# Performance work log

Measured on AMD Instinct MI355X. Metric: run time of the kernel, lower is better.

## Reference

```python
import jax, jax.numpy as jnp
import numpy as np

B = 32768
N_KPS = 14
DIM = N_KPS * 3   # 42
H1 = 1024
N_DOF = 7

# Fixed kinematic-chain constants (stand-in for the robot's link geometry,
# Franka-like link lengths; constants on device in the original).
LINK_LEN = jnp.array([0.333, 0.316, 0.384, 0.088, 0.107, 0.103, 0.100], dtype=jnp.float32)
OFF = jnp.array([0.05, 0.0, 0.0], dtype=jnp.float32)  # per-link auxiliary keypoint offset


def _rot_z(t):
    c, s = jnp.cos(t), jnp.sin(t)
    z, o = jnp.zeros_like(t), jnp.ones_like(t)
    return jnp.stack([jnp.stack([c, -s, z], -1),
                      jnp.stack([s, c, z], -1),
                      jnp.stack([z, z, o], -1)], -2)


def _rot_y(t):
    c, s = jnp.cos(t), jnp.sin(t)
    z, o = jnp.zeros_like(t), jnp.ones_like(t)
    return jnp.stack([jnp.stack([c, z, s], -1),
                      jnp.stack([z, o, z], -1),
                      jnp.stack([-s, z, c], -1)], -2)


def compute_3n_loss_42_rob(angles):
    """Forward kinematics: angles [B,7] -> keypoints [B,14,3].
    Alternating z/y revolute joints; 2 keypoints per link (origin + offset)."""
    Bn = angles.shape[0]
    R = jnp.broadcast_to(jnp.eye(3, dtype=angles.dtype), (Bn, 3, 3))
    p = jnp.zeros((Bn, 3), dtype=angles.dtype)
    pts = []
    for j in range(N_DOF):
        Rj = _rot_z(angles[:, j]) if j % 2 == 0 else _rot_y(angles[:, j])
        R = jnp.einsum('bij,bjk->bik', R, Rj)
        p = p + R @ jnp.array([0.0, 0.0, 1.0], dtype=angles.dtype) * LINK_LEN[j]
        pts.append(p)
        pts.append(p + R @ OFF)
    return jnp.stack(pts, axis=1)  # [B, 14, 3]


def compute_rede_rt(P, Q):
    """Batched Kabsch: rigid (R, t) minimizing ||R P + t - Q||. P,Q: [B,N,3]."""
    cp = P.mean(axis=1, keepdims=True)
    cq = Q.mean(axis=1, keepdims=True)
    H = jnp.einsum('bni,bnj->bij', P - cp, Q - cq)  # [B,3,3]
    U, S, Vt = jnp.linalg.svd(H)
    V = jnp.swapaxes(Vt, -1, -2)
    d = jnp.sign(jnp.linalg.det(jnp.einsum('bij,bkj->bik', V, U)))
    D = jnp.concatenate([jnp.ones((P.shape[0], 2), P.dtype), d[:, None]], axis=1)
    R = jnp.einsum('bij,bj,bkj->bik', V, D, U)  # V diag(1,1,d) U^T
    t = cq[:, 0] - jnp.einsum('bij,bj->bi', R, cp[:, 0])
    return R, t


def setup_inputs() -> dict:
    key = jax.random.key(0)
    k1, k2, k3, k4, k5 = jax.random.split(key, 5)
    return {
        'joints_3d_pred': jax.random.normal(k1, (B, N_KPS, 3), dtype=jnp.float32),
        'W1': jax.random.normal(k2, (DIM, H1), dtype=jnp.float32) * 0.05,
        'b1': jax.random.normal(k3, (H1,), dtype=jnp.float32) * 0.01,
        'W2': jax.random.normal(k4, (H1, N_DOF), dtype=jnp.float32) * 0.05,
        'b2': jax.random.normal(k5, (N_DOF,), dtype=jnp.float32) * 0.01,
    }


def reference(joints_3d_pred, W1, b1, W2, b2):
    # normalize to root keypoint
    norm = joints_3d_pred - joints_3d_pred[:, :1, :]          # [B,14,3]
    x = norm.reshape(norm.shape[0], -1)                        # [B,42]
    h = jax.nn.relu(x @ W1 + b1)                               # [B,1024]
    angles = h @ W2 + b2                                       # [B,7]
    all_dof_pred = angles[:, :, None]                          # [B,7,1]
    rob = compute_3n_loss_42_rob(angles)                       # [B,14,3]
    R, t = compute_rede_rt(rob, norm)
    t = t + joints_3d_pred[:, 0]                               # un-normalize translation
    top = jnp.concatenate([R, t[:, :, None]], axis=2)          # [B,3,4]
    bottom = jnp.broadcast_to(jnp.array([0.0, 0.0, 0.0, 1.0], dtype=R.dtype), (R.shape[0], 1, 4))
    pose = jnp.concatenate([top, bottom], axis=1)              # [B,4,4]
    return all_dof_pred, pose
```

## Files before the change

### kernel.cpp

```cpp
#include <hip/hip_runtime.h>
#include <math.h>

typedef __attribute__((ext_vector_type(8))) _Float16 half8;
typedef __attribute__((ext_vector_type(4))) _Float16 half4;
typedef __attribute__((ext_vector_type(2))) __fp16   fp16x2;
typedef __attribute__((ext_vector_type(4))) float f32x4;

constexpr int B_   = 32768;
constexpr int NKPS = 14;
constexpr int DIM  = 42;
constexpr int H1_  = 1024;
constexpr int NDOF = 7;

__device__ __forceinline__ void gload_lds16(const _Float16* g, _Float16* l) {
    __builtin_amdgcn_global_load_lds(
        (const __attribute__((address_space(1))) void*)g,
        (__attribute__((address_space(3))) void*)l,
        16, 0, 0);
}

__global__ __launch_bounds__(256)
void prep_kernel(const float* __restrict__ W1, const float* __restrict__ b1,
                 const float* __restrict__ W2,
                 _Float16* __restrict__ B1f,
                 _Float16* __restrict__ W2Th, _Float16* __restrict__ W2Tl)
{
    const int T = blockIdx.x * 256 + threadIdx.x;
    if (T < 16384) {
        const int lane  = T & 63;
        const int frag  = T >> 6;
        const int ks    = frag & 3;
        const int ntile = frag >> 2;
        const int n     = ntile * 16 + (lane & 15);
        const int kbase = ks * 32 + ((lane >> 4) << 3);
        half8 s;
#pragma unroll
        for (int j = 0; j < 8; ++j) {
            const int k = kbase + j;
            _Float16 hv;
            if (k < 42) {
                hv = (_Float16)W1[k * H1_ + n];
            } else if (k < 84) {
                hv = (_Float16)W1[(k - 42) * H1_ + n];
            } else if (k < 126) {
                const float x = W1[(k - 84) * H1_ + n];
                const _Float16 hi = (_Float16)x;
                hv = (_Float16)(x - (float)hi);
            } else if (k == 126) {
                hv = (_Float16)b1[n];
            } else {
                const float x = b1[n];
                const _Float16 hi = (_Float16)x;
                hv = (_Float16)(x - (float)hi);
            }
            s[j] = hv;
        }
        *((half8*)(B1f + (long)T * 8)) = s;
    } else if (T < 16384 + 4096) {
        const int idx   = T - 16384;
        const int lane  = idx & 63;
        const int ntile = idx >> 6;
        const int d     = lane & 15;
        const int g     = lane >> 4;
        half4 sh, sl;
#pragma unroll
        for (int j = 0; j < 4; ++j) {
            const int n = ntile * 16 + g * 4 + j;
            float v = (d < 7) ? W2[n * 7 + d] : 0.0f;
            const _Float16 hi = (_Float16)v;
            sh[j] = hi;
            sl[j] = (_Float16)(v - (float)hi);
        }
        *((half4*)(W2Th + (long)idx * 4)) = sh;
        *((half4*)(W2Tl + (long)idx * 4)) = sl;
    }
}

__global__ __launch_bounds__(512, 2)
void mlp_kernel(const float* __restrict__ joints,
                const _Float16* __restrict__ B1f,
                const _Float16* __restrict__ W2Th,
                const _Float16* __restrict__ W2Tl,
                float* __restrict__ pang)
{
    __shared__ __align__(16) _Float16 Bq[32768];
    __shared__ __align__(16) _Float16 W2sh[4096];
    __shared__ __align__(16) _Float16 W2sl[4096];

    const int  tid  = threadIdx.x;
    const int  lane = tid & 63;
    const int  w    = tid >> 6;
    const int  g    = lane >> 4;
    const int  lm   = lane & 15;
    const int  nq   = blockIdx.x & 3;
    const int  rg   = blockIdx.x >> 2;
    const long bm   = (long)rg * 512;

    {
        const _Float16* gs = B1f + (long)nq * 32768 + w * 4096 + lane * 8;
        _Float16* ld = Bq + w * 4096;
#pragma unroll
        for (int i = 0; i < 8; ++i)
            gload_lds16(gs + i * 512, ld + i * 512);
    }
    gload_lds16(W2Th + (long)nq * 4096 + w * 512 + lane * 8, W2sh + w * 512);
    gload_lds16(W2Tl + (long)nq * 4096 + w * 512 + lane * 8, W2sl + w * 512);

    half8 a[4][4];
#pragma unroll
    for (int mt = 0; mt < 4; ++mt) {
        const float* jr = joints + (bm + w * 64 + mt * 16 + lm) * DIM;
        const float q0 = jr[0], q1 = jr[1], q2 = jr[2];
#pragma unroll
        for (int ks = 0; ks < 4; ++ks) {
            half8 s;
#pragma unroll
            for (int j = 0; j < 8; ++j) {
                const int k  = ks * 32 + g * 8 + j;
                const int t1 = (k >= 42) ? 1 : 0;
                const int t2 = (k >= 84) ? 1 : 0;
                int ksrc = k - 42 * (t1 + t2);
                const int m3 = ksrc - 3 * ((ksrc * 21846) >> 16);
                const float x0 = (m3 == 0) ? q0 : ((m3 == 1) ? q1 : q2);
                if (ksrc > 41) ksrc = 41;
                const float xv = jr[ksrc] - x0;
                const _Float16 fh = (_Float16)xv;
                const _Float16 fl = (_Float16)(xv - (float)fh);
                _Float16 r = (t1 && !t2) ? fl : fh;
                if (k >= 126) r = (_Float16)1.0f;
                s[j] = r;
            }
            a[mt][ks] = s;
        }
    }
    __syncthreads();

    f32x4 D2[4];
#pragma unroll
    for (int mt = 0; mt < 4; ++mt) D2[mt] = (f32x4){0.f, 0.f, 0.f, 0.f};

#pragma unroll
    for (int nt = 0; nt < 16; ++nt) {
        half8 bfr[4];
#pragma unroll
        for (int ks = 0; ks < 4; ++ks)
            bfr[ks] = *((const half8*)&Bq[((nt * 4 + ks) * 64 + lane) * 8]);
        const half4 wth = *((const half4*)&W2sh[(nt * 64 + lane) * 4]);
        const half4 wtl = *((const half4*)&W2sl[(nt * 64 + lane) * 4]);

#pragma unroll
        for (int mt = 0; mt < 4; ++mt) {
            f32x4 acc = (f32x4){0.f, 0.f, 0.f, 0.f};
#pragma unroll
            for (int ks = 0; ks < 4; ++ks)
                acc = __builtin_amdgcn_mfma_f32_16x16x32_f16(bfr[ks], a[mt][ks], acc, 0, 0, 0);

            const float h0 = fmaxf(acc[0], 0.f);
            const float h1 = fmaxf(acc[1], 0.f);
            const float h2 = fmaxf(acc[2], 0.f);
            const float h3 = fmaxf(acc[3], 0.f);
            const fp16x2 p01 = __builtin_amdgcn_cvt_pkrtz(h0, h1);
            const fp16x2 p23 = __builtin_amdgcn_cvt_pkrtz(h2, h3);
            half4 bhi;
            bhi[0] = (_Float16)p01[0]; bhi[1] = (_Float16)p01[1];
            bhi[2] = (_Float16)p23[0]; bhi[3] = (_Float16)p23[1];
            const float l0 = h0 - (float)bhi[0];
            const float l1 = h1 - (float)bhi[1];
            const float l2 = h2 - (float)bhi[2];
            const float l3 = h3 - (float)bhi[3];
            const fp16x2 q01 = __builtin_amdgcn_cvt_pkrtz(l0, l1);
            const fp16x2 q23 = __builtin_amdgcn_cvt_pkrtz(l2, l3);
            half4 blo;
            blo[0] = (_Float16)q01[0]; blo[1] = (_Float16)q01[1];
            blo[2] = (_Float16)q23[0]; blo[3] = (_Float16)q23[1];

            D2[mt] = __builtin_amdgcn_mfma_f32_16x16x16f16(wth, bhi, D2[mt], 0, 0, 0);
            D2[mt] = __builtin_amdgcn_mfma_f32_16x16x16f16(wth, blo, D2[mt], 0, 0, 0);
            D2[mt] = __builtin_amdgcn_mfma_f32_16x16x16f16(wtl, bhi, D2[mt], 0, 0, 0);
        }
    }

    if (g < 2) {
#pragma unroll
        for (int mt = 0; mt < 4; ++mt) {
            const long row = bm + w * 64 + mt * 16 + lm;
            *((f32x4*)(pang + ((long)nq * B_ + row) * 8 + g * 4)) = D2[mt];
        }
    }
}

#define JROT(app, aqq, apq, arp, arq, v0p, v0q, v1p, v1q, v2p, v2q) do { \
    double _apq = (apq); \
    if (fabs(_apq) > 1e-300) { \
        double _tau = ((aqq) - (app)) / (2.0 * _apq); \
        double _t = ((_tau >= 0.0) ? 1.0 : -1.0) / (fabs(_tau) + sqrt(1.0 + _tau*_tau)); \
        double _c = 1.0 / sqrt(1.0 + _t*_t); \
        double _s = _t * _c; \
        (app) -= _t * _apq; \
        (aqq) += _t * _apq; \
        (apq) = 0.0; \
        { double _rp = (arp), _rq = (arq); \
          (arp) = _c*_rp - _s*_rq; (arq) = _s*_rp + _c*_rq; } \
        { double _v = (v0p); (v0p) = _c*_v - _s*(v0q); (v0q) = _s*_v + _c*(v0q); } \
        { double _v = (v1p); (v1p) = _c*_v - _s*(v1q); (v1q) = _s*_v + _c*(v1q); } \
        { double _v = (v2p); (v2p) = _c*_v - _s*(v2q); (v2q) = _s*_v + _c*(v2q); } \
    } \
} while (0)

#define SWAP_EIG(ea, eb, va0, vb0, va1, vb1, va2, vb2) do { \
    double _tm; \
    _tm = (ea); (ea) = (eb); (eb) = _tm; \
    _tm = (va0); (va0) = (vb0); (vb0) = _tm; \
    _tm = (va1); (va1) = (vb1); (vb1) = _tm; \
    _tm = (va2); (va2) = (vb2); (vb2) = _tm; \
} while (0)

__global__ __launch_bounds__(128)
void fk_kernel(const float* __restrict__ joints,
               const float* __restrict__ pang,
               const float* __restrict__ b2,
               float* __restrict__ out)
{
    const int b = blockIdx.x * 128 + threadIdx.x;
    if (b >= B_) return;

    const float* jr = joints + (long)b * DIM;
    const float j0x = jr[0], j0y = jr[1], j0z = jr[2];
    float q[DIM];
#pragma unroll
    for (int k = 0; k < NKPS; ++k) {
        q[3*k+0] = jr[3*k+0] - j0x;
        q[3*k+1] = jr[3*k+1] - j0y;
        q[3*k+2] = jr[3*k+2] - j0z;
    }

    float ang[NDOF];
#pragma unroll
    for (int d = 0; d < NDOF; ++d)
        ang[d] = pang[((long)0 * B_ + b) * 8 + d]
               + pang[((long)1 * B_ + b) * 8 + d]
               + pang[((long)2 * B_ + b) * 8 + d]
               + pang[((long)3 * B_ + b) * 8 + d]
               + b2[d];

#pragma unroll
    for (int d = 0; d < NDOF; ++d) out[(long)b * NDOF + d] = ang[d];

    float R00=1.f,R01=0.f,R02=0.f, R10=0.f,R11=1.f,R12=0.f, R20=0.f,R21=0.f,R22=1.f;
    float px=0.f, py=0.f, pz=0.f;
    float Hr00=0.f,Hr01=0.f,Hr02=0.f,Hr10=0.f,Hr11=0.f,Hr12=0.f,Hr20=0.f,Hr21=0.f,Hr22=0.f;
    float sPx=0.f, sPy=0.f, sPz=0.f;
    const float LL[NDOF] = {0.333f,0.316f,0.384f,0.088f,0.107f,0.103f,0.1f};

#pragma unroll
    for (int j = 0; j < NDOF; ++j) {
        float s, c;
        sincosf(ang[j], &s, &c);
        if ((j & 1) == 0) {
            float a0=R00, a1=R01; R00 = c*a0 + s*a1; R01 = c*a1 - s*a0;
            float b0=R10, b1v=R11; R10 = c*b0 + s*b1v; R11 = c*b1v - s*b0;
            float c0=R20, c1=R21; R20 = c*c0 + s*c1; R21 = c*c1 - s*c0;
        } else {
            float a0=R00, a2=R02; R00 = c*a0 - s*a2; R02 = s*a0 + c*a2;
            float b0=R10, b2v=R12; R10 = c*b0 - s*b2v; R12 = s*b0 + c*b2v;
            float c0=R20, c2=R22; R20 = c*c0 - s*c2; R22 = s*c0 + c*c2;
        }
        px = fmaf(LL[j], R02, px);
        py = fmaf(LL[j], R12, py);
        pz = fmaf(LL[j], R22, pz);
        {
            const float qx = q[6*j+0], qy = q[6*j+1], qz = q[6*j+2];
            sPx += px; sPy += py; sPz += pz;
            Hr00 = fmaf(px, qx, Hr00); Hr01 = fmaf(px, qy, Hr01); Hr02 = fmaf(px, qz, Hr02);
            Hr10 = fmaf(py, qx, Hr10); Hr11 = fmaf(py, qy, Hr11); Hr12 = fmaf(py, qz, Hr12);
            Hr20 = fmaf(pz, qx, Hr20); Hr21 = fmaf(pz, qy, Hr21); Hr22 = fmaf(pz, qz, Hr22);
        }
        {
            const float ox = fmaf(0.05f, R00, px);
            const float oy = fmaf(0.05f, R10, py);
            const float oz = fmaf(0.05f, R20, pz);
            const float qx = q[6*j+3], qy = q[6*j+4], qz = q[6*j+5];
            sPx += ox; sPy += oy; sPz += oz;
            Hr00 = fmaf(ox, qx, Hr00); Hr01 = fmaf(ox, qy, Hr01); Hr02 = fmaf(ox, qz, Hr02);
            Hr10 = fmaf(oy, qx, Hr10); Hr11 = fmaf(oy, qy, Hr11); Hr12 = fmaf(oy, qz, Hr12);
            Hr20 = fmaf(oz, qx, Hr20); Hr21 = fmaf(oz, qy, Hr21); Hr22 = fmaf(oz, qz, Hr22);
        }
    }

    float sQx = 0.f, sQy = 0.f, sQz = 0.f;
#pragma unroll
    for (int n = 0; n < NKPS; ++n) { sQx += q[3*n+0]; sQy += q[3*n+1]; sQz += q[3*n+2]; }

    const double inv14 = 1.0 / 14.0;
    const double cpx = (double)sPx * inv14, cpy = (double)sPy * inv14, cpz = (double)sPz * inv14;
    const double cqx = (double)sQx * inv14, cqy = (double)sQy * inv14, cqz = (double)sQz * inv14;

    const double h00 = (double)Hr00 - 14.0*cpx*cqx, h01 = (double)Hr01 - 14.0*cpx*cqy, h02 = (double)Hr02 - 14.0*cpx*cqz;
    const double h10 = (double)Hr10 - 14.0*cpy*cqx, h11 = (double)Hr11 - 14.0*cpy*cqy, h12 = (double)Hr12 - 14.0*cpy*cqz;
    const double h20 = (double)Hr20 - 14.0*cpz*cqx, h21 = (double)Hr21 - 14.0*cpz*cqy, h22 = (double)Hr22 - 14.0*cpz*cqz;

    double m00 = h00*h00 + h10*h10 + h20*h20;
    double m01 = h00*h01 + h10*h11 + h20*h21;
    double m02 = h00*h02 + h10*h12 + h20*h22;
    double m11 = h01*h01 + h11*h11 + h21*h21;
    double m12 = h01*h02 + h11*h12 + h21*h22;
    double m22 = h02*h02 + h12*h12 + h22*h22;

    double v00=1.0, v01=0.0, v02=0.0;
    double v10=0.0, v11=1.0, v12=0.0;
    double v20=0.0, v21=0.0, v22=1.0;

#pragma unroll
    for (int sw = 0; sw < 5; ++sw) {
        JROT(m00, m11, m01, m02, m12, v00, v01, v10, v11, v20, v21);
        JROT(m00, m22, m02, m01, m12, v00, v02, v10, v12, v20, v22);
        JROT(m11, m22, m12, m01, m02, v01, v02, v11, v12, v21, v22);
    }

    double e0 = m00, e1 = m11, e2 = m22;
    if (e0 < e1) SWAP_EIG(e0, e1, v00, v01, v10, v11, v20, v21);
    if (e0 < e2) SWAP_EIG(e0, e2, v00, v02, v10, v12, v20, v22);
    if (e1 < e2) SWAP_EIG(e1, e2, v01, v02, v11, v12, v21, v22);

    const double s0 = sqrt(fmax(e0, 0.0));
    const double s1 = sqrt(fmax(e1, 0.0));
    const double s2 = sqrt(fmax(e2, 0.0));

    const double det = h00*(h11*h22 - h12*h21) - h01*(h10*h22 - h12*h20) + h02*(h10*h21 - h11*h20);
    const double dsg = (det >= 0.0) ? 1.0 : -1.0;

    const double tiny = 1e-30;
    const double g0 = 1.0 / fmax(s0, tiny);
    const double g1 = 1.0 / fmax(s1, tiny);
    const double g2 = dsg / fmax(s2, tiny);

    const double K00 = g0*v00*v00 + g1*v01*v01 + g2*v02*v02;
    const double K01 = g0*v00*v10 + g1*v01*v11 + g2*v02*v12;
    const double K02 = g0*v00*v20 + g1*v01*v21 + g2*v02*v22;
    const double K11 = g0*v10*v10 + g1*v11*v11 + g2*v12*v12;
    const double K12 = g0*v10*v20 + g1*v11*v21 + g2*v12*v22;
    const double K22 = g0*v20*v20 + g1*v21*v21 + g2*v22*v22;

    const double r00 = K00*h00 + K01*h01 + K02*h02;
    const double r01 = K00*h10 + K01*h11 + K02*h12;
    const double r02 = K00*h20 + K01*h21 + K02*h22;
    const double r10 = K01*h00 + K11*h01 + K12*h02;
    const double r11 = K01*h10 + K11*h11 + K12*h12;
    const double r12 = K01*h20 + K11*h21 + K12*h22;
    const double r20 = K02*h00 + K12*h01 + K22*h02;
    const double r21 = K02*h10 + K12*h11 + K22*h12;
    const double r22 = K02*h20 + K12*h21 + K22*h22;

    const double tx = cqx - (r00*cpx + r01*cpy + r02*cpz) + (double)j0x;
    const double ty = cqy - (r10*cpx + r11*cpy + r12*cpz) + (double)j0y;
    const double tz = cqz - (r20*cpx + r21*cpy + r22*cpz) + (double)j0z;

    float* po = out + (long)B_ * NDOF + (long)b * 16;
    po[0]  = (float)r00; po[1]  = (float)r01; po[2]  = (float)r02; po[3]  = (float)tx;
    po[4]  = (float)r10; po[5]  = (float)r11; po[6]  = (float)r12; po[7]  = (float)ty;
    po[8]  = (float)r20; po[9]  = (float)r21; po[10] = (float)r22; po[11] = (float)tz;
    po[12] = 0.f; po[13] = 0.f; po[14] = 0.f; po[15] = 1.f;
}

extern "C" void kernel_launch(void* const* d_in, const int* in_sizes, int n_in,
                              void* d_out, int out_size, void* d_ws, size_t ws_size,
                              hipStream_t stream) {
    const float* joints = (const float*)d_in[0];
    const float* W1     = (const float*)d_in[1];
    const float* b1     = (const float*)d_in[2];
    const float* W2     = (const float*)d_in[3];
    const float* b2     = (const float*)d_in[4];
    float* out = (float*)d_out;

    _Float16* B1f  = (_Float16*)d_ws;
    _Float16* W2Th = (_Float16*)((char*)d_ws + 262144);
    _Float16* W2Tl = (_Float16*)((char*)d_ws + 294912);
    float*    pang = (float*)((char*)d_ws + 327680);

    hipLaunchKernelGGL(prep_kernel, dim3(80), dim3(256), 0, stream,
                       W1, b1, W2, B1f, W2Th, W2Tl);

    hipLaunchKernelGGL(mlp_kernel, dim3(256), dim3(512), 0, stream,
                       joints, B1f, W2Th, W2Tl, pang);

    hipLaunchKernelGGL(fk_kernel, dim3(B_ / 128), dim3(128), 0, stream,
                       joints, pang, b2, out);
}
```

Baseline: 43.24 us.

## Split MLP hidden dim into eight slices and use smaller row tiles

Result: slower. 44.73 us (+3.4%).

```diff
diff --git a/kernel.cpp b/kernel.cpp
--- a/kernel.cpp
+++ b/kernel.cpp
@@ -83,64 +83,71 @@
                 const _Float16* __restrict__ W2Tl,
                 float* __restrict__ pang)
 {
-    __shared__ __align__(16) _Float16 Bq[32768];
-    __shared__ __align__(16) _Float16 W2sh[4096];
-    __shared__ __align__(16) _Float16 W2sl[4096];
+    __shared__ __align__(16) _Float16 Bq[16384];
+    __shared__ __align__(16) _Float16 W2sh[2048];
+    __shared__ __align__(16) _Float16 W2sl[2048];
+    __shared__ __align__(16) float    Jl[128 * DIM];
 
     const int  tid  = threadIdx.x;
     const int  lane = tid & 63;
     const int  w    = tid >> 6;
     const int  g    = lane >> 4;
     const int  lm   = lane & 15;
-    const int  nq   = blockIdx.x & 3;
-    const int  rg   = blockIdx.x >> 2;
-    const long bm   = (long)rg * 512;
+    const int  e    = blockIdx.x & 7;
+    const int  rg   = blockIdx.x >> 3;
+    const long bm   = (long)rg * 128;
 
     {
-        const _Float16* gs = B1f + (long)nq * 32768 + w * 4096 + lane * 8;
-        _Float16* ld = Bq + w * 4096;
-#pragma unroll
-        for (int i = 0; i < 8; ++i)
+        const _Float16* gs = B1f + (long)e * 16384 + w * 2048 + lane * 8;
+        _Float16* ld = Bq + w * 2048;
+#pragma unroll
+        for (int i = 0; i < 4; ++i)
             gload_lds16(gs + i * 512, ld + i * 512);
     }
-    gload_lds16(W2Th + (long)nq * 4096 + w * 512 + lane * 8, W2sh + w * 512);
-    gload_lds16(W2Tl + (long)nq * 4096 + w * 512 + lane * 8, W2sl + w * 512);
-
-    half8 a[4][4];
-#pragma unroll
-    for (int mt = 0; mt < 4; ++mt) {
-        const float* jr = joints + (bm + w * 64 + mt * 16 + lm) * DIM;
-        const float q0 = jr[0], q1 = jr[1], q2 = jr[2];
-#pragma unroll
-        for (int ks = 0; ks < 4; ++ks) {
-            half8 s;
-#pragma unroll
-            for (int j = 0; j < 8; ++j) {
-                const int k  = ks * 32 + g * 8 + j;
-                const int t1 = (k >= 42) ? 1 : 0;
-                const int t2 = (k >= 84) ? 1 : 0;
-                int ksrc = k - 42 * (t1 + t2);
-                const int m3 = ksrc - 3 * ((ksrc * 21846) >> 16);
-                const float x0 = (m3 == 0) ? q0 : ((m3 == 1) ? q1 : q2);
-                if (ksrc > 41) ksrc = 41;
-                const float xv = jr[ksrc] - x0;
-                const _Float16 fh = (_Float16)xv;
-                const _Float16 fl = (_Float16)(xv - (float)fh);
-                _Float16 r = (t1 && !t2) ? fl : fh;
-                if (k >= 126) r = (_Float16)1.0f;
-                s[j] = r;
-            }
-            a[mt][ks] = s;
+    if (w < 4)
+        gload_lds16(W2Th + (long)e * 2048 + w * 512 + lane * 8, W2sh + w * 512);
+    else
+        gload_lds16(W2Tl + (long)e * 2048 + (w - 4) * 512 + lane * 8, W2sl + (w - 4) * 512);
+
+    {
+        const f32x4* jg = (const f32x4*)(joints + bm * DIM);
+#pragma unroll
+        for (int i = 0; i < 3; ++i) {
+            const int idx = i * 512 + tid;
+            if (idx < 1344) ((f32x4*)Jl)[idx] = jg[idx];
         }
     }
     __syncthreads();
 
-    f32x4 D2[4];
-#pragma unroll
-    for (int mt = 0; mt < 4; ++mt) D2[mt] = (f32x4){0.f, 0.f, 0.f, 0.f};
-
-#pragma unroll
-    for (int nt = 0; nt < 16; ++nt) {
+    const int   lrow = w * 16 + lm;
+    const float* jr  = Jl + lrow * DIM;
+    const float q0 = jr[0], q1 = jr[1], q2 = jr[2];
+    half8 a[4];
+#pragma unroll
+    for (int ks = 0; ks < 4; ++ks) {
+        half8 s;
+#pragma unroll
+        for (int j = 0; j < 8; ++j) {
+            const int k  = ks * 32 + g * 8 + j;
+            const int t1 = (k >= 42) ? 1 : 0;
+            const int t2 = (k >= 84) ? 1 : 0;
+            int ksrc = k - 42 * (t1 + t2);
+            const int m3 = ksrc - 3 * ((ksrc * 21846) >> 16);
+            const float x0 = (m3 == 0) ? q0 : ((m3 == 1) ? q1 : q2);
+            if (ksrc > 41) ksrc = 41;
+            const float xv = jr[ksrc] - x0;
+            const _Float16 fh = (_Float16)xv;
+            const _Float16 fl = (_Float16)(xv - (float)fh);
+            _Float16 r = (t1 && !t2) ? fl : fh;
+            if (k >= 126) r = (_Float16)1.0f;
+            s[j] = r;
+        }
+        a[ks] = s;
+    }
+
+    f32x4 D2 = (f32x4){0.f, 0.f, 0.f, 0.f};
+#pragma unroll
+    for (int nt = 0; nt < 8; ++nt) {
         half8 bfr[4];
 #pragma unroll
         for (int ks = 0; ks < 4; ++ks)
@@ -148,44 +155,38 @@
         const half4 wth = *((const half4*)&W2sh[(nt * 64 + lane) * 4]);
         const half4 wtl = *((const half4*)&W2sl[(nt * 64 + lane) * 4]);
 
-#pragma unroll
-        for (int mt = 0; mt < 4; ++mt) {
-            f32x4 acc = (f32x4){0.f, 0.f, 0.f, 0.f};
-#pragma unroll
-            for (int ks = 0; ks < 4; ++ks)
-                acc = __builtin_amdgcn_mfma_f32_16x16x32_f16(bfr[ks], a[mt][ks], acc, 0, 0, 0);
-
-            const float h0 = fmaxf(acc[0], 0.f);
-            const float h1 = fmaxf(acc[1], 0.f);
-            const float h2 = fmaxf(acc[2], 0.f);
-            const float h3 = fmaxf(acc[3], 0.f);
-            const fp16x2 p01 = __builtin_amdgcn_cvt_pkrtz(h0, h1);
-            const fp16x2 p23 = __builtin_amdgcn_cvt_pkrtz(h2, h3);
-            half4 bhi;
-            bhi[0] = (_Float16)p01[0]; bhi[1] = (_Float16)p01[1];
-            bhi[2] = (_Float16)p23[0]; bhi[3] = (_Float16)p23[1];
-            const float l0 = h0 - (float)bhi[0];
-            const float l1 = h1 - (float)bhi[1];
-            const float l2 = h2 - (float)bhi[2];
-            const float l3 = h3 - (float)bhi[3];
-            const fp16x2 q01 = __builtin_amdgcn_cvt_pkrtz(l0, l1);
-            const fp16x2 q23 = __builtin_amdgcn_cvt_pkrtz(l2, l3);
-            half4 blo;
-            blo[0] = (_Float16)q01[0]; blo[1] = (_Float16)q01[1];
-            blo[2] = (_Float16)q23[0]; blo[3] = (_Float16)q23[1];
-
-            D2[mt] = __builtin_amdgcn_mfma_f32_16x16x16f16(wth, bhi, D2[mt], 0, 0, 0);
-            D2[mt] = __builtin_amdgcn_mfma_f32_16x16x16f16(wth, blo, D2[mt], 0, 0, 0);
-            D2[mt] = __builtin_amdgcn_mfma_f32_16x16x16f16(wtl, bhi, D2[mt], 0, 0, 0);
-        }
+        f32x4 acc = (f32x4){0.f, 0.f, 0.f, 0.f};
+#pragma unroll
+        for (int ks = 0; ks < 4; ++ks)
+            acc = __builtin_amdgcn_mfma_f32_16x16x32_f16(bfr[ks], a[ks], acc, 0, 0, 0);
+
+        const float h0 = fmaxf(acc[0], 0.f);
+        const float h1 = fmaxf(acc[1], 0.f);
+        const float h2 = fmaxf(acc[2], 0.f);
+        const float h3 = fmaxf(acc[3], 0.f);
+        const fp16x2 p01 = __builtin_amdgcn_cvt_pkrtz(h0, h1);
+        const fp16x2 p23 = __builtin_amdgcn_cvt_pkrtz(h2, h3);
+        half4 bhi;
+        bhi[0] = (_Float16)p01[0]; bhi[1] = (_Float16)p01[1];
+        bhi[2] = (_Float16)p23[0]; bhi[3] = (_Float16)p23[1];
+        const float l0 = h0 - (float)bhi[0];
+        const float l1 = h1 - (float)bhi[1];
+        const float l2 = h2 - (float)bhi[2];
+        const float l3 = h3 - (float)bhi[3];
+        const fp16x2 q01 = __builtin_amdgcn_cvt_pkrtz(l0, l1);
+        const fp16x2 q23 = __builtin_amdgcn_cvt_pkrtz(l2, l3);
+        half4 blo;
+        blo[0] = (_Float16)q01[0]; blo[1] = (_Float16)q01[1];
+        blo[2] = (_Float16)q23[0]; blo[3] = (_Float16)q23[1];
+
+        D2 = __builtin_amdgcn_mfma_f32_16x16x16f16(wth, bhi, D2, 0, 0, 0);
+        D2 = __builtin_amdgcn_mfma_f32_16x16x16f16(wth, blo, D2, 0, 0, 0);
+        D2 = __builtin_amdgcn_mfma_f32_16x16x16f16(wtl, bhi, D2, 0, 0, 0);
     }
 
     if (g < 2) {
-#pragma unroll
-        for (int mt = 0; mt < 4; ++mt) {
-            const long row = bm + w * 64 + mt * 16 + lm;
-            *((f32x4*)(pang + ((long)nq * B_ + row) * 8 + g * 4)) = D2[mt];
-        }
+        const long row = bm + lrow;
+        *((f32x4*)(pang + ((long)e * B_ + row) * 8 + g * 4)) = D2;
     }
 }
 
@@ -234,14 +235,18 @@
         q[3*k+2] = jr[3*k+2] - j0z;
     }
 
+    f32x4 s0 = (f32x4){0.f, 0.f, 0.f, 0.f};
+    f32x4 s1 = (f32x4){0.f, 0.f, 0.f, 0.f};
+#pragma unroll
+    for (int e = 0; e < 8; ++e) {
+        s0 += *((const f32x4*)(pang + ((long)e * B_ + b) * 8));
+        s1 += *((const f32x4*)(pang + ((long)e * B_ + b) * 8 + 4));
+    }
     float ang[NDOF];
-#pragma unroll
-    for (int d = 0; d < NDOF; ++d)
-        ang[d] = pang[((long)0 * B_ + b) * 8 + d]
-               + pang[((long)1 * B_ + b) * 8 + d]
-               + pang[((long)2 * B_ + b) * 8 + d]
-               + pang[((long)3 * B_ + b) * 8 + d]
-               + b2[d];
+    ang[0] = s0[0] + b2[0]; ang[1] = s0[1] + b2[1];
+    ang[2] = s0[2] + b2[2]; ang[3] = s0[3] + b2[3];
+    ang[4] = s1[0] + b2[4]; ang[5] = s1[1] + b2[5];
+    ang[6] = s1[2] + b2[6];
 
 #pragma unroll
     for (int d = 0; d < NDOF; ++d) out[(long)b * NDOF + d] = ang[d];
@@ -322,17 +327,17 @@
     if (e0 < e2) SWAP_EIG(e0, e2, v00, v02, v10, v12, v20, v22);
     if (e1 < e2) SWAP_EIG(e1, e2, v01, v02, v11, v12, v21, v22);
 
-    const double s0 = sqrt(fmax(e0, 0.0));
-    const double s1 = sqrt(fmax(e1, 0.0));
-    const double s2 = sqrt(fmax(e2, 0.0));
+    const double s0v = sqrt(fmax(e0, 0.0));
+    const double s1v = sqrt(fmax(e1, 0.0));
+    const double s2v = sqrt(fmax(e2, 0.0));
 
     const double det = h00*(h11*h22 - h12*h21) - h01*(h10*h22 - h12*h20) + h02*(h10*h21 - h11*h20);
     const double dsg = (det >= 0.0) ? 1.0 : -1.0;
 
     const double tiny = 1e-30;
-    const double g0 = 1.0 / fmax(s0, tiny);
-    const double g1 = 1.0 / fmax(s1, tiny);
-    const double g2 = dsg / fmax(s2, tiny);
+    const double g0 = 1.0 / fmax(s0v, tiny);
+    const double g1 = 1.0 / fmax(s1v, tiny);
+    const double g2 = dsg / fmax(s2v, tiny);
 
     const double K00 = g0*v00*v00 + g1*v01*v01 + g2*v02*v02;
     const double K01 = g0*v00*v10 + g1*v01*v11 + g2*v02*v12;
@@ -380,7 +385,7 @@
     hipLaunchKernelGGL(prep_kernel, dim3(80), dim3(256), 0, stream,
                        W1, b1, W2, B1f, W2Th, W2Tl);
 
-    hipLaunchKernelGGL(mlp_kernel, dim3(256), dim3(512), 0, stream,
+    hipLaunchKernelGGL(mlp_kernel, dim3(2048), dim3(512), 0, stream,
                        joints, B1f, W2Th, W2Tl, pang);
 
     hipLaunchKernelGGL(fk_kernel, dim3(B_ / 128), dim3(128), 0, stream,
```
